# Optimization experiments

Measured on AMD Instinct MI355X. Metric: run time of the kernel, lower is better.

Reference implementation:

```python
import jax, jax.numpy as jnp
import numpy as np

BELIEF = 1024
STOCH = 32
DISC = 32
LATENT = 1024
MLP = 1024
ACT = 6
B = 256
T = 64
UNIMIX = 0.01
FREE = 0.1
DYN_SCALE = 1.0
REP_SCALE = 0.1
EPS = 1e-8
SAMP_EPS = 1e-6
CLIP = 20.0
UPDATE_BIAS = -1.0


def _lin_init(key, fan_in, fan_out):
    return jax.random.normal(key, (fan_in, fan_out), jnp.float32) / np.sqrt(fan_in)


def setup_inputs() -> dict:
    key = jax.random.key(0)
    ks = jax.random.split(key, 16)
    inp = {
        "b0": jnp.zeros((B, BELIEF), jnp.float32),
        "z0": jax.random.uniform(ks[0], (B, STOCH * DISC), jnp.float32),
        "actions": jax.random.normal(ks[1], (T, B, ACT), jnp.float32),
        "obs": jax.random.normal(ks[2], (T, B, LATENT), jnp.float32),
        "u_noise": jax.random.uniform(ks[3], (T, B, STOCH, DISC), jnp.float32),
        # imagine_in MLP: (stoch*disc + act) -> MLP -> LATENT
        "Wi1": _lin_init(ks[4], STOCH * DISC + ACT, MLP),
        "bi1": jnp.zeros((MLP,), jnp.float32),
        "Wi2": _lin_init(ks[5], MLP, LATENT),
        "bi2": jnp.zeros((LATENT,), jnp.float32),
        # GRU linear: (LATENT + BELIEF) -> 3*BELIEF, no bias; LayerNorm(3*BELIEF, eps=1e-3)
        "Wg": _lin_init(ks[6], LATENT + BELIEF, 3 * BELIEF),
        "ln_scale": jnp.ones((3 * BELIEF,), jnp.float32),
        "ln_bias": jnp.zeros((3 * BELIEF,), jnp.float32),
        # posterior MLP: (LATENT + BELIEF) -> LATENT -> STOCH*DISC
        "Wo1": _lin_init(ks[7], LATENT + BELIEF, LATENT),
        "bo1": jnp.zeros((LATENT,), jnp.float32),
        "Wo2": _lin_init(ks[8], LATENT, STOCH * DISC),
        "bo2": jnp.zeros((STOCH * DISC,), jnp.float32),
        # prior (belief decoder) MLP: BELIEF -> LATENT -> STOCH*DISC
        "Wp1": _lin_init(ks[9], BELIEF, LATENT),
        "bp1": jnp.zeros((LATENT,), jnp.float32),
        "Wp2": _lin_init(ks[10], LATENT, STOCH * DISC),
        "bp2": jnp.zeros((STOCH * DISC,), jnp.float32),
    }
    return inp


def _mlp2(x, W1, b1, W2, b2):
    h = jax.nn.silu(x @ W1 + b1)
    return h @ W2 + b2


def _layernorm(x, scale, bias, eps=1e-3):
    mu = x.mean(-1, keepdims=True)
    var = ((x - mu) ** 2).mean(-1, keepdims=True)
    return (x - mu) / jnp.sqrt(var + eps) * scale + bias


def _probs_from_logits(logits_flat):
    # reshape (..., STOCH*DISC) -> (..., STOCH, DISC), clip, softmax, unimix
    logits = logits_flat.reshape(*logits_flat.shape[:-1], STOCH, DISC)
    logits = jnp.clip(logits, -CLIP, CLIP)
    probs = jax.nn.softmax(logits, axis=-1)
    probs = probs * (1.0 - UNIMIX) + UNIMIX / DISC
    return probs


def _kl_cate(post_probs, prior_probs):
    sg = jax.lax.stop_gradient
    log_post = jnp.log(post_probs + EPS)
    kl_rep = (post_probs * (log_post - jnp.log(sg(prior_probs) + EPS))).sum((-2, -1))
    kl_dyn = (sg(post_probs) * (sg(log_post) - jnp.log(prior_probs + EPS))).sum((-2, -1))
    rep_loss = jnp.maximum(kl_rep, FREE)
    dyn_loss = jnp.maximum(kl_dyn, FREE)
    return DYN_SCALE * dyn_loss + REP_SCALE * rep_loss


def reference(b0, z0, actions, obs, u_noise,
              Wi1, bi1, Wi2, bi2,
              Wg, ln_scale, ln_bias,
              Wo1, bo1, Wo2, bo2,
              Wp1, bp1, Wp2, bp2):
    def gru(inp, h):
        gates = _layernorm(jnp.concatenate([inp, h], axis=-1) @ Wg, ln_scale, ln_bias)
        r, c, u = jnp.split(gates, 3, axis=-1)
        reset = jax.nn.sigmoid(r)
        cand = jnp.tanh(reset * c)
        update = jax.nn.sigmoid(u + UPDATE_BIAS)
        return update * cand + (1.0 - update) * h

    def step(carry, xs):
        b, z = carry
        a_t, o_t, u_t = xs
        inp = _mlp2(jnp.concatenate([z, a_t], axis=-1), Wi1, bi1, Wi2, bi2)
        b_new = gru(inp, b)                                      # (B, BELIEF)
        prior_probs = _probs_from_logits(_mlp2(b_new, Wp1, bp1, Wp2, bp2))
        post_probs = _probs_from_logits(
            _mlp2(jnp.concatenate([o_t, b_new], axis=-1), Wo1, bo1, Wo2, bo2))
        # gumbel-max categorical sample + straight-through one-hot
        g = -jnp.log(-jnp.log(u_t + SAMP_EPS) + SAMP_EPS)
        logp = jnp.log(jnp.maximum(post_probs, SAMP_EPS))
        hard = jnp.argmax(logp + g, axis=-1)                     # (B, STOCH)
        y_hard = jax.nn.one_hot(hard, DISC, dtype=post_probs.dtype)
        z_st = y_hard + post_probs - jax.lax.stop_gradient(post_probs)
        z_flat = z_st.reshape(z_st.shape[0], STOCH * DISC)
        loss = _kl_cate(post_probs, prior_probs)                 # (B,)
        return (b_new, z_flat), loss

    (_, _), losses = jax.lax.scan(step, (b0, z0), (actions, obs, u_noise))
    return losses  # (T, B)
```

## Files before the change

### kernel.cpp

```cpp
#include <hip/hip_runtime.h>
#include <math.h>


typedef _Float16 f16;
typedef _Float16 f16x8 __attribute__((ext_vector_type(8)));
typedef float f32x4 __attribute__((ext_vector_type(4)));

constexpr int kB = 256, kN1 = 1024, kG3N = 3072, kActD = 6, kT = 64;
constexpr float kLoScale = 4096.f;
constexpr float kLoInv = 1.f / 4096.f;

__device__ __forceinline__ float lda_sc(const float* p) {
  return __hip_atomic_load(p, __ATOMIC_RELAXED, __HIP_MEMORY_SCOPE_AGENT);
}
__device__ __forceinline__ void stg_sc(float* p, float v) {
  __hip_atomic_store(p, v, __ATOMIC_RELAXED, __HIP_MEMORY_SCOPE_AGENT);
}
__device__ __forceinline__ int aadd(int* p, int v) {
  return __hip_atomic_fetch_add(p, v, __ATOMIC_RELAXED, __HIP_MEMORY_SCOPE_AGENT);
}
__device__ __forceinline__ int ald(int* p) {
  return __hip_atomic_load(p, __ATOMIC_RELAXED, __HIP_MEMORY_SCOPE_AGENT);
}

__device__ __forceinline__ void wr_planes(f16* hi, f16* lo, size_t i, float x) {
  f16 h = (f16)x;
  hi[i] = h;
  lo[i] = (f16)((x - (float)h) * kLoScale);
}

__device__ __forceinline__ void glds16(const f16* g, f16* l) {
  __builtin_amdgcn_global_load_lds(
      (const __attribute__((address_space(1))) unsigned int*)g,
      (__attribute__((address_space(3))) unsigned int*)l, 16, 0, 0);
}

struct GemmLDS  { f16 As[3][2][8][64][8]; f16 Ws[3][2][4][64][8]; };
struct Gemm2LDS { f16 As[2][2][8][64][8]; f16 Ws[2][2][8][64][8]; };
struct GruLDS  { float sh[kG3N]; float red[8]; };
struct SmpLDS  { float skl[32]; int sidx[32]; };
union GGLDS { Gemm2LDS g; GruLDS r; };
union ESLDS { Gemm2LDS g; SmpLDS s; };

__device__ void dev_mgemm2(Gemm2LDS& L, const f16* A1h, const f16* A1l,
                           const f16* A2h, const f16* A2l,
                           const f16* Wph, const f16* Wpl, float* outF,
                           int cols1, int K, int Nout, int k0, int klen,
                           int bx, int byp, int pstride, int pidx) {
  const int m0 = bx * 128, n0 = byp * 128;
  const int tid = threadIdx.x, wave = tid >> 6, lane = tid & 63;
  const int rlo = lane & 15, khi = (lane >> 4) * 8;
  const int wmf = (wave & 1) * 4, wnf = (wave >> 1) * 4;

  f32x4 acc1[4][4], acc2[4][4];
#pragma unroll
  for (int i = 0; i < 4; ++i)
#pragma unroll
    for (int j = 0; j < 4; ++j)
#pragma unroll
      for (int r = 0; r < 4; ++r) { acc1[i][j][r] = 0.f; acc2[i][j][r] = 0.f; }

  auto issueTile = [&](int it, int buf) {
    const int kg = k0 + it * 32;
    const f16 *h, *l; int rs, cb;
    if (kg < cols1) { h = A1h; l = A1l; rs = cols1; cb = kg; }
    else { h = A2h; l = A2l; rs = K - cols1; cb = kg - cols1; }
#pragma unroll
    for (int i = 0; i < 2; ++i) {
      const int mf = wave * 2 + i;
      const size_t go = (size_t)(m0 + mf * 16 + rlo) * rs + cb + khi;
      glds16(h + go, &L.As[buf][0][mf][0][0]);
      glds16(l + go, &L.As[buf][1][mf][0][0]);
    }
#pragma unroll
    for (int i = 0; i < 2; ++i) {
      const int p = wave * 2 + i;
      const size_t wo = (size_t)(n0 + p * 16 + rlo) * K + kg + khi;
      glds16(Wph + wo, &L.Ws[buf][0][p][0][0]);
      glds16(Wpl + wo, &L.Ws[buf][1][p][0][0]);
    }
  };

  const int niter = klen >> 5;
  issueTile(0, 0);
#pragma unroll 1
  for (int it = 0; it < niter; ++it) {
    const int buf = it & 1;
    if (it + 1 < niter) {
      issueTile(it + 1, buf ^ 1);
      asm volatile("s_waitcnt vmcnt(8)" ::: "memory");
    } else {
      asm volatile("s_waitcnt vmcnt(0)" ::: "memory");
    }
    __builtin_amdgcn_s_barrier();
    asm volatile("" ::: "memory");
    f16x8 Af[4][2], Wf[4][2];
#pragma unroll
    for (int mf = 0; mf < 4; ++mf) {
      Af[mf][0] = *(const f16x8*)&L.As[buf][0][wmf + mf][lane][0];
      Af[mf][1] = *(const f16x8*)&L.As[buf][1][wmf + mf][lane][0];
    }
#pragma unroll
    for (int nf = 0; nf < 4; ++nf) {
      Wf[nf][0] = *(const f16x8*)&L.Ws[buf][0][wnf + nf][lane][0];
      Wf[nf][1] = *(const f16x8*)&L.Ws[buf][1][wnf + nf][lane][0];
    }
#pragma unroll
    for (int mf = 0; mf < 4; ++mf)
#pragma unroll
      for (int nf = 0; nf < 4; ++nf) {
        acc1[mf][nf] = __builtin_amdgcn_mfma_f32_16x16x32_f16(Af[mf][0], Wf[nf][0], acc1[mf][nf], 0, 0, 0);
        acc2[mf][nf] = __builtin_amdgcn_mfma_f32_16x16x32_f16(Af[mf][0], Wf[nf][1], acc2[mf][nf], 0, 0, 0);
        acc2[mf][nf] = __builtin_amdgcn_mfma_f32_16x16x32_f16(Af[mf][1], Wf[nf][0], acc2[mf][nf], 0, 0, 0);
      }
    __builtin_amdgcn_s_barrier();
  }
  __syncthreads();
  const int orow = m0 + (wave & 1) * 64, ocol = n0 + (wave >> 1) * 64;
#pragma unroll
  for (int mf = 0; mf < 4; ++mf)
#pragma unroll
    for (int nf = 0; nf < 4; ++nf)
#pragma unroll
      for (int r = 0; r < 4; ++r) {
        const int row = orow + mf * 16 + (lane >> 4) * 4 + r;
        const int col = ocol + nf * 16 + rlo;
        const int o = row * Nout + col;
        float* dst = outF + ((size_t)(o >> 4) * pstride + pidx) * 16 + (o & 15);
        stg_sc(dst, acc1[mf][nf][r] + acc2[mf][nf][r] * kLoInv);
      }
}

__device__ void dev_mgemm(GemmLDS& L, const f16* A1h, const f16* A1l,
                          const f16* A2h, const f16* A2l,
                          const f16* Wph, const f16* Wpl, float* outF,
                          int cols1, int K, int Nout, int k0, int klen,
                          int bx, int by, int pstride, int pidx) {
  const int m0 = bx * 128, n0 = by * 64;
  const int tid = threadIdx.x, wave = tid >> 6, lane = tid & 63;
  const int rlo = lane & 15, khi = (lane >> 4) * 8;
  const int wmf = (wave & 1) * 4, wnf = (wave >> 1) * 2;

  f32x4 acc1[4][2], acc2[4][2];
#pragma unroll
  for (int i = 0; i < 4; ++i)
#pragma unroll
    for (int j = 0; j < 2; ++j)
#pragma unroll
      for (int r = 0; r < 4; ++r) { acc1[i][j][r] = 0.f; acc2[i][j][r] = 0.f; }

  auto issueTile = [&](int it, int buf) {
    const int kg = k0 + it * 32;
    const f16 *h, *l; int rs, cb;
    if (kg < cols1) { h = A1h; l = A1l; rs = cols1; cb = kg; }
    else { h = A2h; l = A2l; rs = K - cols1; cb = kg - cols1; }
#pragma unroll
    for (int i = 0; i < 2; ++i) {
      const int mf = wave * 2 + i;
      const size_t go = (size_t)(m0 + mf * 16 + rlo) * rs + cb + khi;
      glds16(h + go, &L.As[buf][0][mf][0][0]);
      glds16(l + go, &L.As[buf][1][mf][0][0]);
    }
    const size_t wo = (size_t)(n0 + wave * 16 + rlo) * K + kg + khi;
    glds16(Wph + wo, &L.Ws[buf][0][wave][0][0]);
    glds16(Wpl + wo, &L.Ws[buf][1][wave][0][0]);
  };

  const int niter = klen >> 5;
  issueTile(0, 0);
  if (niter > 1) issueTile(1, 1);
#pragma unroll 1
  for (int it = 0; it < niter; ++it) {
    const int buf = it % 3;
    if (it + 1 < niter) {
      asm volatile("s_waitcnt vmcnt(6)" ::: "memory");
    } else {
      asm volatile("s_waitcnt vmcnt(0)" ::: "memory");
    }
    __builtin_amdgcn_s_barrier();
    asm volatile("" ::: "memory");
    if (it + 2 < niter) issueTile(it + 2, (it + 2) % 3);
    f16x8 Af[4][2], Wf[2][2];
#pragma unroll
    for (int mf = 0; mf < 4; ++mf) {
      Af[mf][0] = *(const f16x8*)&L.As[buf][0][wmf + mf][lane][0];
      Af[mf][1] = *(const f16x8*)&L.As[buf][1][wmf + mf][lane][0];
    }
#pragma unroll
    for (int nf = 0; nf < 2; ++nf) {
      Wf[nf][0] = *(const f16x8*)&L.Ws[buf][0][wnf + nf][lane][0];
      Wf[nf][1] = *(const f16x8*)&L.Ws[buf][1][wnf + nf][lane][0];
    }
#pragma unroll
    for (int mf = 0; mf < 4; ++mf)
#pragma unroll
      for (int nf = 0; nf < 2; ++nf) {
        acc1[mf][nf] = __builtin_amdgcn_mfma_f32_16x16x32_f16(Af[mf][0], Wf[nf][0], acc1[mf][nf], 0, 0, 0);
        acc2[mf][nf] = __builtin_amdgcn_mfma_f32_16x16x32_f16(Af[mf][0], Wf[nf][1], acc2[mf][nf], 0, 0, 0);
        acc2[mf][nf] = __builtin_amdgcn_mfma_f32_16x16x32_f16(Af[mf][1], Wf[nf][0], acc2[mf][nf], 0, 0, 0);
      }
  }
  __syncthreads();
  const int orow = m0 + (wave & 1) * 64, ocol = n0 + (wave >> 1) * 32;
#pragma unroll
  for (int mf = 0; mf < 4; ++mf)
#pragma unroll
    for (int nf = 0; nf < 2; ++nf)
#pragma unroll
      for (int r = 0; r < 4; ++r) {
        const int row = orow + mf * 16 + (lane >> 4) * 4 + r;
        const int col = ocol + nf * 16 + rlo;
        const int o = row * Nout + col;
        float* dst = outF + ((size_t)(o >> 4) * pstride + pidx) * 16 + (o & 15);
        stg_sc(dst, acc1[mf][nf][r] + acc2[mf][nf][r] * kLoInv);
      }
}

__device__ __forceinline__ void flag_bump(int* ctr) {
  asm volatile("s_waitcnt vmcnt(0)" ::: "memory");
  __syncthreads();
  if (threadIdx.x == 0) aadd(ctr, 1);
}
__device__ __forceinline__ void spin_ge(int* p, int tgt) {
  if (threadIdx.x == 0) {
    int guard = 0;
    while (ald(p) < tgt) {
      __builtin_amdgcn_s_sleep(4);
      if (++guard > (1 << 17)) break;
    }
  }
  __syncthreads();
}

__device__ __forceinline__ int permW(int B2, int pairsPerCls) {
  const int cls = B2 & 7, k = B2 >> 3;
  return ((cls * pairsPerCls + (k >> 1)) << 1) | (k & 1);
}

struct GGArgs {
  const f16 *h1h, *h1l, *bh_r, *bl_r;
  const f16 *WfTh, *WfTl, *WgBh, *WgBl;
  float* Pg;
  const float *bfused, *lns, *lnb, *obs;
  float* bbuf;
  f16 *bh_w, *bl_w, *onh, *onl;
  int* ctr;
  int t;
};

__global__ __launch_bounds__(256, 2) void k_gates_gru(GGArgs a) {
  __shared__ GGLDS L;
  const int t = a.t;
  if (blockIdx.x < 192) {
    const int task = permW(blockIdx.x, 12);
    const int j = task / 48, r = task % 48, bx = r & 1, byp = r >> 1;
    const bool top = (j < 2);
    dev_mgemm2(L.g, top ? a.h1h : a.bh_r, top ? a.h1l : a.bl_r, nullptr, nullptr,
               top ? a.WfTh : a.WgBh, top ? a.WfTl : a.WgBl,
               a.Pg, 1024, 1024, kG3N, (j & 1) * 512, 512, bx, byp, 4, j);
    flag_bump(a.ctr + bx * 16);
  }
  const int b = blockIdx.x;
  if (b >= kB) return;
  spin_ge(a.ctr + (b >> 7) * 16, (t + 1) * 96);

  GruLDS& G = L.r;
  const int tid = threadIdx.x;
  float v[12];
  float sum = 0.f, sq = 0.f;
#pragma unroll
  for (int i = 0; i < 12; ++i) {
    const int j = tid + i * 256;
    const size_t o = (size_t)b * kG3N + j;
    const float* base = a.Pg + ((o >> 4) * 4) * 16 + (o & 15);
    const float q0 = lda_sc(base),      q1 = lda_sc(base + 16);
    const float q2 = lda_sc(base + 32), q3 = lda_sc(base + 48);
    const float s = (((q0 + q1) + q2) + q3) + a.bfused[j];
    v[i] = s; sum += s; sq += s * s;
  }
  if (t < kT - 1) {
#pragma unroll
    for (int i = 0; i < 4; ++i) {
      const int j = tid + i * 256;
      wr_planes(a.onh, a.onl, (size_t)b * kN1 + j,
                a.obs[(size_t)(t + 1) * kB * kN1 + (size_t)b * kN1 + j]);
    }
  }
  for (int m = 1; m <= 32; m <<= 1) { sum += __shfl_xor(sum, m); sq += __shfl_xor(sq, m); }
  if ((tid & 63) == 0) { G.red[(tid >> 6) * 2] = sum; G.red[(tid >> 6) * 2 + 1] = sq; }
  __syncthreads();
  float ts = 0.f, tq = 0.f;
  for (int w = 0; w < 4; ++w) { ts += G.red[w * 2]; tq += G.red[w * 2 + 1]; }
  const float mu   = ts * (1.f / kG3N);
  const float var  = tq * (1.f / kG3N) - mu * mu;
  const float rinv = 1.f / sqrtf(var + 1e-3f);
#pragma unroll
  for (int i = 0; i < 12; ++i) {
    const int j = tid + i * 256;
    G.sh[j] = (v[i] - mu) * rinv * a.lns[j] + a.lnb[j];
  }
  __syncthreads();
#pragma unroll
  for (int i = 0; i < 4; ++i) {
    const int j = tid + i * 256;
    const float r = G.sh[j], c = G.sh[kN1 + j], u = G.sh[2 * kN1 + j];
    const float reset = 1.f / (1.f + expf(-r));
    const float cand  = tanhf(reset * c);
    const float upd   = 1.f / (1.f + expf(-(u - 1.f)));
    const size_t o = (size_t)b * kN1 + j;
    const float bn = upd * cand + (1.f - upd) * a.bbuf[o];
    a.bbuf[o] = bn;
    wr_planes(a.bh_w, a.bl_w, o, bn);
  }
}

struct DCArgs {
  const f16 *bh, *bl, *oth, *otl;
  const f16 *Wp1Th, *Wp1Tl, *Wo1Th, *Wo1Tl;
  float* PD;
  const float *bp1, *bo1;
  f16 *hph, *hpl, *hoh, *hol;
  int* ctr;
  int t;
};

__global__ __launch_bounds__(256, 2) void k_d_comb(DCArgs a) {
  __shared__ Gemm2LDS L;
  const int t = a.t;
  if (blockIdx.x < 96) {
    const int task = permW(blockIdx.x, 6);
    const int j = task >> 4, r = task & 15, bx = r & 1, byp = r >> 1;
    const f16 *Ah, *Al, *A2h = nullptr, *A2l = nullptr, *Wh, *Wl;
    int K, k0;
    if (j < 2) { Ah = a.bh; Al = a.bl; Wh = a.Wp1Th; Wl = a.Wp1Tl; K = 1024; k0 = j * 512; }
    else { Ah = a.oth; Al = a.otl; A2h = a.bh; A2l = a.bl; Wh = a.Wo1Th; Wl = a.Wo1Tl; K = 2048; k0 = (j - 2) * 512; }
    dev_mgemm2(L, Ah, Al, A2h, A2l, Wh, Wl, a.PD, 1024, K, kN1, k0, 512, bx, byp, 6, j);
    flag_bump(a.ctr + bx * 16);
  }
  spin_ge(a.ctr, (t + 1) * 48);
  spin_ge(a.ctr + 16, (t + 1) * 48);
#pragma unroll 1
  for (int idx = blockIdx.x; idx < 1024; idx += 192) {
    const int i = idx * 256 + (int)threadIdx.x;
    const float* base = a.PD + ((size_t)(i >> 4) * 6) * 16 + (i & 15);
    const float p0 = lda_sc(base),      p1 = lda_sc(base + 16);
    const float p2 = lda_sc(base + 32), p3 = lda_sc(base + 48);
    const float p4 = lda_sc(base + 64), p5 = lda_sc(base + 80);
    float sp = (p0 + p1) + a.bp1[i & (kN1 - 1)];
    sp = sp * (1.f / (1.f + expf(-sp)));
    wr_planes(a.hph, a.hpl, i, sp);
    float so = (((p2 + p3) + p4) + p5) + a.bo1[i & (kN1 - 1)];
    so = so * (1.f / (1.f + expf(-so)));
    wr_planes(a.hoh, a.hol, i, so);
  }
}

struct ESArgs {
  const f16 *hph, *hpl, *hoh, *hol;
  const f16 *Wp2Th, *Wp2Tl, *Wo2Th, *Wo2Tl;
  float* PE;
  const float *bp2, *bo2, *unz, *acts, *Wi1, *bi1;
  float* out;
  f16 *h1h, *h1l;
  int* ctr;
  int t;
};

__global__ __launch_bounds__(256, 2) void k_e_samp(ESArgs a) {
  __shared__ ESLDS L;
  const int t = a.t;
  if (blockIdx.x < 64) {
    const int task = permW(blockIdx.x, 4);
    const int j = task >> 4, r = task & 15, bx = r & 1, byp = r >> 1;
    const bool pr = (j < 2);
    dev_mgemm2(L.g, pr ? a.hph : a.hoh, pr ? a.hpl : a.hol, nullptr, nullptr,
               pr ? a.Wp2Th : a.Wo2Th, pr ? a.Wp2Tl : a.Wo2Tl,
               a.PE, 1024, 1024, kN1, (j & 1) * 512, 512, bx, byp, 4, j);
    flag_bump(a.ctr + bx * 16);
  }
  const int b = blockIdx.x;
  spin_ge(a.ctr + (b >> 7) * 16, (t + 1) * 32);

  SmpLDS& S = L.s;
  const int tid = threadIdx.x;
  const float* unz_t = a.unz + (size_t)t * kB * kN1;
  __syncthreads();
#pragma unroll
  for (int c = 0; c < 4; ++c) {
    const int j = c * 256 + tid;
    const int o = b * kN1 + j;
    const float* base = a.PE + ((size_t)(o >> 4) * 4) * 16 + (o & 15);
    const float e0 = lda_sc(base),      e1 = lda_sc(base + 16);
    const float e2 = lda_sc(base + 32), e3 = lda_sc(base + 48);
    float lp = e0 + e1 + a.bp2[j];
    float lo = e2 + e3 + a.bo2[j];
    lp = fminf(fmaxf(lp, -20.f), 20.f);
    lo = fminf(fmaxf(lo, -20.f), 20.f);
    float mp = lp, mo = lo;
    for (int m = 1; m <= 16; m <<= 1) { mp = fmaxf(mp, __shfl_xor(mp, m)); mo = fmaxf(mo, __shfl_xor(mo, m)); }
    const float ep = expf(lp - mp), eo = expf(lo - mo);
    float sp = ep, so = eo;
    for (int m = 1; m <= 16; m <<= 1) { sp += __shfl_xor(sp, m); so += __shfl_xor(so, m); }
    const float pp = (ep / sp) * 0.99f + (0.01f / 32.f);
    const float po = (eo / so) * 0.99f + (0.01f / 32.f);
    float kt = po * (logf(po + 1e-8f) - logf(pp + 1e-8f));
    for (int m = 1; m <= 16; m <<= 1) kt += __shfl_xor(kt, m);
    const float u = unz_t[o];
    const float g = -logf(-logf(u + 1e-6f) + 1e-6f);
    float vv = logf(fmaxf(po, 1e-6f)) + g;
    int ii = j & 31;
    for (int m = 1; m <= 16; m <<= 1) {
      const float vo = __shfl_xor(vv, m);
      const int   io = __shfl_xor(ii, m);
      if (vo > vv || (vo == vv && io < ii)) { vv = vo; ii = io; }
    }
    if ((tid & 31) == 0) { S.skl[j >> 5] = kt; S.sidx[j >> 5] = ii; }
  }
  __syncthreads();
  if (tid == 0) {
    float kl = 0.f;
    for (int gg = 0; gg < 32; ++gg) kl += S.skl[gg];
    const float dl = fmaxf(kl, 0.1f);
    a.out[(size_t)t * kB + b] = 1.0f * dl + 0.1f * dl;
  }
  if (t < kT - 1) {
    const float* act_next = a.acts + (size_t)(t + 1) * kB * kActD;
#pragma unroll
    for (int c = 0; c < 4; ++c) {
      const int j = c * 256 + tid;
      float s = a.bi1[j];
#pragma unroll
      for (int gg = 0; gg < 32; ++gg)
        s += a.Wi1[(size_t)(gg * 32 + S.sidx[gg]) * kN1 + j];
#pragma unroll
      for (int k = 0; k < kActD; ++k)
        s += act_next[b * kActD + k] * a.Wi1[(size_t)(kN1 + k) * kN1 + j];
      s = s * (1.f / (1.f + expf(-s)));
      wr_planes(a.h1h, a.h1l, (size_t)b * kN1 + j, s);
    }
  }
}

struct MJob {
  const f16 *A1h, *A1l, *A2h, *A2l;
  const f16 *Wph, *Wpl;
  float* outF;
  int cols1, K, Nout, k0, klen, ny, pstride, pidx;
};
struct MJobs { MJob j[6]; };

__global__ __launch_bounds__(256, 2) void k_mgemm(MJobs js) {
  const MJob jb = js.j[blockIdx.z];
  if ((int)blockIdx.y >= jb.ny) return;
  __shared__ GemmLDS L;
  dev_mgemm(L, jb.A1h, jb.A1l, jb.A2h, jb.A2l, jb.Wph, jb.Wpl, jb.outF,
            jb.cols1, jb.K, jb.Nout, jb.k0, jb.klen, blockIdx.x, blockIdx.y,
            jb.pstride, jb.pidx);
}

__global__ __launch_bounds__(256) void k_conv(const float* src, f16* dh, f16* dl) {
  const size_t i = (size_t)blockIdx.x * 256 + threadIdx.x;
  wr_planes(dh, dl, i, src[i]);
}

__global__ __launch_bounds__(256) void k_convT(const float* src, int rowoff, int srcN,
                                               int K, f16* dh, f16* dl) {
  __shared__ float T[64][65];
  const int k0 = blockIdx.x * 64, n0 = blockIdx.y * 64;
  const int tx = threadIdx.x & 63, ty = threadIdx.x >> 6;
#pragma unroll 4
  for (int i = 0; i < 16; ++i) {
    const int k = ty * 16 + i;
    T[k][tx] = src[(size_t)(rowoff + k0 + k) * srcN + n0 + tx];
  }
  __syncthreads();
#pragma unroll 4
  for (int i = 0; i < 16; ++i) {
    const int n = ty * 16 + i;
    const float x = T[tx][n];
    const size_t o = (size_t)(n0 + n) * K + k0 + tx;
    f16 h = (f16)x;
    dh[o] = h;
    dl[o] = (f16)((x - (float)h) * kLoScale);
  }
}

__global__ __launch_bounds__(256) void k_bfused(const float* Wg, const float* bi2, float* bf) {
  const int n = blockIdx.x * 256 + threadIdx.x;
  float s = 0.f;
#pragma unroll 16
  for (int j = 0; j < 1024; ++j) s += bi2[j] * Wg[(size_t)j * kG3N + n];
  bf[n] = s;
}

__global__ __launch_bounds__(256) void k_setup(const float* b0, float* bbuf, f16* bh, f16* bl) {
  const size_t i = (size_t)blockIdx.x * 256 + threadIdx.x;
  const float b = b0[i];
  bbuf[i] = b;
  wr_planes(bh, bl, i, b);
}

__global__ void k_zero(int* p) {
  const int i = blockIdx.x * 256 + threadIdx.x;
  if (i < 512) p[i] = 0;
}

__global__ __launch_bounds__(256) void k_finish0(const float* P, const float* Wi1,
    const float* bi1, const float* act0, f16* h1h, f16* h1l) {
  const int b = blockIdx.y;
  const int j = blockIdx.x * 256 + threadIdx.x;
  __shared__ float sact[kActD];
  if (threadIdx.x < kActD) sact[threadIdx.x] = act0[b * kActD + threadIdx.x];
  __syncthreads();
  float s = P[(size_t)b * kN1 + j] + bi1[j];
#pragma unroll
  for (int k = 0; k < kActD; ++k) s += sact[k] * Wi1[(size_t)(kN1 + k) * kN1 + j];
  s = s * (1.f / (1.f + expf(-s)));
  wr_planes(h1h, h1l, (size_t)b * kN1 + j, s);
}

extern "C" void kernel_launch(void* const* d_in, const int* in_sizes, int n_in,
                              void* d_out, int out_size, void* d_ws, size_t ws_size,
                              hipStream_t stream) {
  const float* b0   = (const float*)d_in[0];
  const float* z0   = (const float*)d_in[1];
  const float* acts = (const float*)d_in[2];
  const float* obs  = (const float*)d_in[3];
  const float* unz  = (const float*)d_in[4];
  const float* Wi1  = (const float*)d_in[5];
  const float* bi1  = (const float*)d_in[6];
  const float* Wi2  = (const float*)d_in[7];
  const float* bi2  = (const float*)d_in[8];
  const float* Wg   = (const float*)d_in[9];
  const float* lns  = (const float*)d_in[10];
  const float* lnb  = (const float*)d_in[11];
  const float* Wo1  = (const float*)d_in[12];
  const float* bo1  = (const float*)d_in[13];
  const float* Wo2  = (const float*)d_in[14];
  const float* bo2  = (const float*)d_in[15];
  const float* Wp1  = (const float*)d_in[16];
  const float* bp1  = (const float*)d_in[17];
  const float* Wp2  = (const float*)d_in[18];
  const float* bp2  = (const float*)d_in[19];
  float* out = (float*)d_out;

  char* wsb = (char*)d_ws;
  size_t off = 0;
  auto allocB = [&](size_t bytes) { char* p = wsb + off; off += (bytes + 255) & ~(size_t)255; return p; };
  const size_t PL = (size_t)kB * kN1;
  const size_t S3 = (size_t)kB * kG3N;
  const size_t W1 = (size_t)kN1 * kN1;

  float* Pg = (float*)allocB(4 * S3 * 4);
  float* Wfused_tmp = Pg;
  f16* WgTh = (f16*)allocB(W1 * 3 * 2);
  f16* WgTl = (f16*)allocB(W1 * 3 * 2);
  float* PD = (float*)WgTh;
  float* PE = (float*)WgTl;
  f16* h1h = (f16*)allocB(PL * 2);  f16* h1l = (f16*)allocB(PL * 2);
  f16* bh  = (f16*)allocB(PL * 2);  f16* bl  = (f16*)allocB(PL * 2);
  f16* hph = (f16*)allocB(PL * 2);  f16* hpl = (f16*)allocB(PL * 2);
  f16* hoh = (f16*)allocB(PL * 2);  f16* hol = (f16*)allocB(PL * 2);
  f16* o0h = (f16*)allocB(PL * 2);  f16* o0l = (f16*)allocB(PL * 2);
  f16* o1h = (f16*)allocB(PL * 2);  f16* o1l = (f16*)allocB(PL * 2);
  f16* z0h = (f16*)allocB(PL * 2);  f16* z0l = (f16*)allocB(PL * 2);
  float* bbuf   = (float*)allocB(PL * 4);
  float* bfused = (float*)allocB((size_t)kG3N * 4);
  f16* WfTh = (f16*)allocB(W1 * 3 * 2);  f16* WfTl = (f16*)allocB(W1 * 3 * 2);
  f16* WgBh = (f16*)allocB(W1 * 3 * 2);  f16* WgBl = (f16*)allocB(W1 * 3 * 2);
  f16* Wi2h = (f16*)allocB(W1 * 2);      f16* Wi2l = (f16*)allocB(W1 * 2);
  f16* Wi1Th = (f16*)allocB(W1 * 2);     f16* Wi1Tl = (f16*)allocB(W1 * 2);
  f16* Wo1Th = (f16*)allocB(W1 * 2 * 2); f16* Wo1Tl = (f16*)allocB(W1 * 2 * 2);
  f16* Wp1Th = (f16*)allocB(W1 * 2);     f16* Wp1Tl = (f16*)allocB(W1 * 2);
  f16* Wp2Th = (f16*)allocB(W1 * 2);     f16* Wp2Tl = (f16*)allocB(W1 * 2);
  f16* Wo2Th = (f16*)allocB(W1 * 2);     f16* Wo2Tl = (f16*)allocB(W1 * 2);
  int* cnt = (int*)allocB(4096);

  k_convT<<<dim3(16, 48), 256, 0, stream>>>(Wg, 0, kG3N, 1024, WgTh, WgTl);
  k_convT<<<dim3(16, 48), 256, 0, stream>>>(Wg, 1024, kG3N, 1024, WgBh, WgBl);
  k_convT<<<dim3(16, 16), 256, 0, stream>>>(Wi1, 0, kN1, 1024, Wi1Th, Wi1Tl);
  k_convT<<<dim3(32, 16), 256, 0, stream>>>(Wo1, 0, kN1, 2048, Wo1Th, Wo1Tl);
  k_convT<<<dim3(16, 16), 256, 0, stream>>>(Wp1, 0, kN1, 1024, Wp1Th, Wp1Tl);
  k_convT<<<dim3(16, 16), 256, 0, stream>>>(Wp2, 0, kN1, 1024, Wp2Th, Wp2Tl);
  k_convT<<<dim3(16, 16), 256, 0, stream>>>(Wo2, 0, kN1, 1024, Wo2Th, Wo2Tl);
  k_conv<<<dim3(4096), 256, 0, stream>>>(Wi2, Wi2h, Wi2l);
  k_bfused<<<dim3(12), 256, 0, stream>>>(Wg, bi2, bfused);
  {
    MJobs J{};
    J.j[0] = { Wi2h, Wi2l, nullptr, nullptr, WgTh, WgTl, Wfused_tmp, 1024, 1024, kG3N, 0, 1024, 48, 1, 0 };
    k_mgemm<<<dim3(8, 48, 1), 256, 0, stream>>>(J);
  }
  k_convT<<<dim3(16, 48), 256, 0, stream>>>(Wfused_tmp, 0, kG3N, 1024, WfTh, WfTl);
  k_setup<<<dim3(1024), 256, 0, stream>>>(b0, bbuf, bh, bl);
  k_conv<<<dim3(1024), 256, 0, stream>>>(z0, z0h, z0l);
  k_conv<<<dim3(1024), 256, 0, stream>>>(obs, o0h, o0l);
  k_zero<<<dim3(2), 256, 0, stream>>>(cnt);
  {
    MJobs J{};
    J.j[0] = { z0h, z0l, nullptr, nullptr, Wi1Th, Wi1Tl, PD, 1024, 1024, kN1, 0, 1024, 16, 1, 0 };
    k_mgemm<<<dim3(2, 16, 1), 256, 0, stream>>>(J);
  }
  k_finish0<<<dim3(4, kB), 256, 0, stream>>>(PD, Wi1, bi1, acts, h1h, h1l);

  for (int t = 0; t < kT; ++t) {
    f16* oth = (t & 1) ? o1h : o0h;
    f16* otl = (t & 1) ? o1l : o0l;
    f16* onh = (t & 1) ? o0h : o1h;
    f16* onl = (t & 1) ? o0l : o1l;

    GGArgs A;
    A.h1h = h1h; A.h1l = h1l; A.bh_r = bh; A.bl_r = bl;
    A.WfTh = WfTh; A.WfTl = WfTl; A.WgBh = WgBh; A.WgBl = WgBl;
    A.Pg = Pg; A.bfused = bfused; A.lns = lns; A.lnb = lnb; A.obs = obs;
    A.bbuf = bbuf; A.bh_w = bh; A.bl_w = bl; A.onh = onh; A.onl = onl;
    A.ctr = cnt; A.t = t;
    k_gates_gru<<<dim3(256), 256, 0, stream>>>(A);

    DCArgs D;
    D.bh = bh; D.bl = bl; D.oth = oth; D.otl = otl;
    D.Wp1Th = Wp1Th; D.Wp1Tl = Wp1Tl; D.Wo1Th = Wo1Th; D.Wo1Tl = Wo1Tl;
    D.PD = PD; D.bp1 = bp1; D.bo1 = bo1;
    D.hph = hph; D.hpl = hpl; D.hoh = hoh; D.hol = hol;
    D.ctr = cnt + 32; D.t = t;
    k_d_comb<<<dim3(192), 256, 0, stream>>>(D);

    ESArgs E;
    E.hph = hph; E.hpl = hpl; E.hoh = hoh; E.hol = hol;
    E.Wp2Th = Wp2Th; E.Wp2Tl = Wp2Tl; E.Wo2Th = Wo2Th; E.Wo2Tl = Wo2Tl;
    E.PE = PE; E.bp2 = bp2; E.bo2 = bo2; E.unz = unz; E.acts = acts;
    E.Wi1 = Wi1; E.bi1 = bi1; E.out = out; E.h1h = h1h; E.h1l = h1l;
    E.ctr = cnt + 64; E.t = t;
    k_e_samp<<<dim3(256), 256, 0, stream>>>(E);
  }
}
```

Measured before the change: 6.369 ms.

## Precompute obs projection for all steps and drop split-K partial reductions

The observation half of the posterior first-layer GEMM is hoisted out of the recurrence: all timesteps of obs are converted to f16 hi/lo planes and multiplied by the obs slice of Wo1 in one large batched GEMM before the loop. Each per-step GEMM now runs its full K range inside one block with 128x64 tiles, so it writes final outputs directly instead of split-K partials that a second phase had to sum. The posterior/prior first layer kernel no longer needs the counter-spin phase. The cost is fewer active blocks per step (96/64 instead of 192), longer serial K loops per block, and extra workspace for the full-sequence obs buffers.

Measured after the change: 13.59 ms. 113% more time.

```diff
diff --git a/kernel.cpp b/kernel.cpp
--- a/kernel.cpp
+++ b/kernel.cpp
@@ -35,186 +35,101 @@
       (__attribute__((address_space(3))) unsigned int*)l, 16, 0, 0);
 }
 
-struct GemmLDS  { f16 As[3][2][8][64][8]; f16 Ws[3][2][4][64][8]; };
-struct Gemm2LDS { f16 As[2][2][8][64][8]; f16 Ws[2][2][8][64][8]; };
+struct Core16LDS { f16 As[2][2][8][64][8]; f16 Ws[2][2][4][64][8]; };
+struct GemmLDS   { f16 As[3][2][8][64][8]; f16 Ws[3][2][4][64][8]; };
 struct GruLDS  { float sh[kG3N]; float red[8]; };
 struct SmpLDS  { float skl[32]; int sidx[32]; };
-union GGLDS { Gemm2LDS g; GruLDS r; };
-union ESLDS { Gemm2LDS g; SmpLDS s; };
-
-__device__ void dev_mgemm2(Gemm2LDS& L, const f16* A1h, const f16* A1l,
-                           const f16* A2h, const f16* A2l,
-                           const f16* Wph, const f16* Wpl, float* outF,
-                           int cols1, int K, int Nout, int k0, int klen,
-                           int bx, int byp, int pstride, int pidx) {
-  const int m0 = bx * 128, n0 = byp * 128;
+union GGLDS { Core16LDS g; GruLDS r; };
+union ESLDS { Core16LDS g; SmpLDS s; };
+
+__device__ __forceinline__ void gcore16(Core16LDS& L,
+    const f16* Ah, const f16* Al, int rsA,
+    const f16* Wh, const f16* Wl, int KW,
+    int kA, int kW, int m0, int n0,
+    f32x4 (&p)[4][2], bool accum) {
   const int tid = threadIdx.x, wave = tid >> 6, lane = tid & 63;
   const int rlo = lane & 15, khi = (lane >> 4) * 8;
-  const int wmf = (wave & 1) * 4, wnf = (wave >> 1) * 4;
-
-  f32x4 acc1[4][4], acc2[4][4];
+  const int wmf = (wave & 1) * 4, wnf = (wave >> 1) * 2;
+
+  f32x4 acc1[4][2], acc2[4][2];
 #pragma unroll
   for (int i = 0; i < 4; ++i)
 #pragma unroll
-    for (int j = 0; j < 4; ++j)
+    for (int j = 0; j < 2; ++j)
 #pragma unroll
       for (int r = 0; r < 4; ++r) { acc1[i][j][r] = 0.f; acc2[i][j][r] = 0.f; }
 
-  auto issueTile = [&](int it, int buf) {
-    const int kg = k0 + it * 32;
-    const f16 *h, *l; int rs, cb;
-    if (kg < cols1) { h = A1h; l = A1l; rs = cols1; cb = kg; }
-    else { h = A2h; l = A2l; rs = K - cols1; cb = kg - cols1; }
+  auto issue = [&](int it, int buf) {
+    const int kgA = kA + it * 32, kgW = kW + it * 32;
 #pragma unroll
     for (int i = 0; i < 2; ++i) {
       const int mf = wave * 2 + i;
-      const size_t go = (size_t)(m0 + mf * 16 + rlo) * rs + cb + khi;
-      glds16(h + go, &L.As[buf][0][mf][0][0]);
-      glds16(l + go, &L.As[buf][1][mf][0][0]);
-    }
-#pragma unroll
-    for (int i = 0; i < 2; ++i) {
-      const int p = wave * 2 + i;
-      const size_t wo = (size_t)(n0 + p * 16 + rlo) * K + kg + khi;
-      glds16(Wph + wo, &L.Ws[buf][0][p][0][0]);
-      glds16(Wpl + wo, &L.Ws[buf][1][p][0][0]);
-    }
+      const size_t go = (size_t)(m0 + mf * 16 + rlo) * rsA + kgA + khi;
+      glds16(Ah + go, &L.As[buf][0][mf][0][0]);
+      glds16(Al + go, &L.As[buf][1][mf][0][0]);
+    }
+    const size_t wo = (size_t)(n0 + wave * 16 + rlo) * KW + kgW + khi;
+    glds16(Wh + wo, &L.Ws[buf][0][wave][0][0]);
+    glds16(Wl + wo, &L.Ws[buf][1][wave][0][0]);
   };
 
-  const int niter = klen >> 5;
-  issueTile(0, 0);
+  issue(0, 0);
 #pragma unroll 1
-  for (int it = 0; it < niter; ++it) {
+  for (int it = 0; it < 16; ++it) {
     const int buf = it & 1;
-    if (it + 1 < niter) {
-      issueTile(it + 1, buf ^ 1);
-      asm volatile("s_waitcnt vmcnt(8)" ::: "memory");
+    if (it + 1 < 16) {
+      issue(it + 1, buf ^ 1);
+      asm volatile("s_waitcnt vmcnt(6)" ::: "memory");
     } else {
       asm volatile("s_waitcnt vmcnt(0)" ::: "memory");
     }
     __builtin_amdgcn_s_barrier();
     asm volatile("" ::: "memory");
-    f16x8 Af[4][2], Wf[4][2];
+    f16x8 Af[4][2], Wf[2][2];
 #pragma unroll
     for (int mf = 0; mf < 4; ++mf) {
       Af[mf][0] = *(const f16x8*)&L.As[buf][0][wmf + mf][lane][0];
       Af[mf][1] = *(const f16x8*)&L.As[buf][1][wmf + mf][lane][0];
     }
 #pragma unroll
-    for (int nf = 0; nf < 4; ++nf) {
+    for (int nf = 0; nf < 2; ++nf) {
       Wf[nf][0] = *(const f16x8*)&L.Ws[buf][0][wnf + nf][lane][0];
       Wf[nf][1] = *(const f16x8*)&L.Ws[buf][1][wnf + nf][lane][0];
     }
 #pragma unroll
     for (int mf = 0; mf < 4; ++mf)
 #pragma unroll
-      for (int nf = 0; nf < 4; ++nf) {
+      for (int nf = 0; nf < 2; ++nf) {
         acc1[mf][nf] = __builtin_amdgcn_mfma_f32_16x16x32_f16(Af[mf][0], Wf[nf][0], acc1[mf][nf], 0, 0, 0);
         acc2[mf][nf] = __builtin_amdgcn_mfma_f32_16x16x32_f16(Af[mf][0], Wf[nf][1], acc2[mf][nf], 0, 0, 0);
         acc2[mf][nf] = __builtin_amdgcn_mfma_f32_16x16x32_f16(Af[mf][1], Wf[nf][0], acc2[mf][nf], 0, 0, 0);
       }
     __builtin_amdgcn_s_barrier();
   }
-  __syncthreads();
-  const int orow = m0 + (wave & 1) * 64, ocol = n0 + (wave >> 1) * 64;
 #pragma unroll
   for (int mf = 0; mf < 4; ++mf)
 #pragma unroll
-    for (int nf = 0; nf < 4; ++nf)
+    for (int nf = 0; nf < 2; ++nf)
 #pragma unroll
       for (int r = 0; r < 4; ++r) {
-        const int row = orow + mf * 16 + (lane >> 4) * 4 + r;
-        const int col = ocol + nf * 16 + rlo;
-        const int o = row * Nout + col;
-        float* dst = outF + ((size_t)(o >> 4) * pstride + pidx) * 16 + (o & 15);
-        stg_sc(dst, acc1[mf][nf][r] + acc2[mf][nf][r] * kLoInv);
+        const float t = acc1[mf][nf][r] + acc2[mf][nf][r] * kLoInv;
+        p[mf][nf][r] = accum ? (p[mf][nf][r] + t) : t;
       }
 }
 
-__device__ void dev_mgemm(GemmLDS& L, const f16* A1h, const f16* A1l,
-                          const f16* A2h, const f16* A2l,
-                          const f16* Wph, const f16* Wpl, float* outF,
-                          int cols1, int K, int Nout, int k0, int klen,
-                          int bx, int by, int pstride, int pidx) {
-  const int m0 = bx * 128, n0 = by * 64;
-  const int tid = threadIdx.x, wave = tid >> 6, lane = tid & 63;
-  const int rlo = lane & 15, khi = (lane >> 4) * 8;
-  const int wmf = (wave & 1) * 4, wnf = (wave >> 1) * 2;
-
-  f32x4 acc1[4][2], acc2[4][2];
-#pragma unroll
-  for (int i = 0; i < 4; ++i)
-#pragma unroll
-    for (int j = 0; j < 2; ++j)
-#pragma unroll
-      for (int r = 0; r < 4; ++r) { acc1[i][j][r] = 0.f; acc2[i][j][r] = 0.f; }
-
-  auto issueTile = [&](int it, int buf) {
-    const int kg = k0 + it * 32;
-    const f16 *h, *l; int rs, cb;
-    if (kg < cols1) { h = A1h; l = A1l; rs = cols1; cb = kg; }
-    else { h = A2h; l = A2l; rs = K - cols1; cb = kg - cols1; }
-#pragma unroll
-    for (int i = 0; i < 2; ++i) {
-      const int mf = wave * 2 + i;
-      const size_t go = (size_t)(m0 + mf * 16 + rlo) * rs + cb + khi;
-      glds16(h + go, &L.As[buf][0][mf][0][0]);
-      glds16(l + go, &L.As[buf][1][mf][0][0]);
-    }
-    const size_t wo = (size_t)(n0 + wave * 16 + rlo) * K + kg + khi;
-    glds16(Wph + wo, &L.Ws[buf][0][wave][0][0]);
-    glds16(Wpl + wo, &L.Ws[buf][1][wave][0][0]);
-  };
-
-  const int niter = klen >> 5;
-  issueTile(0, 0);
-  if (niter > 1) issueTile(1, 1);
-#pragma unroll 1
-  for (int it = 0; it < niter; ++it) {
-    const int buf = it % 3;
-    if (it + 1 < niter) {
-      asm volatile("s_waitcnt vmcnt(6)" ::: "memory");
-    } else {
-      asm volatile("s_waitcnt vmcnt(0)" ::: "memory");
-    }
-    __builtin_amdgcn_s_barrier();
-    asm volatile("" ::: "memory");
-    if (it + 2 < niter) issueTile(it + 2, (it + 2) % 3);
-    f16x8 Af[4][2], Wf[2][2];
-#pragma unroll
-    for (int mf = 0; mf < 4; ++mf) {
-      Af[mf][0] = *(const f16x8*)&L.As[buf][0][wmf + mf][lane][0];
-      Af[mf][1] = *(const f16x8*)&L.As[buf][1][wmf + mf][lane][0];
-    }
-#pragma unroll
-    for (int nf = 0; nf < 2; ++nf) {
-      Wf[nf][0] = *(const f16x8*)&L.Ws[buf][0][wnf + nf][lane][0];
-      Wf[nf][1] = *(const f16x8*)&L.Ws[buf][1][wnf + nf][lane][0];
-    }
-#pragma unroll
-    for (int mf = 0; mf < 4; ++mf)
-#pragma unroll
-      for (int nf = 0; nf < 2; ++nf) {
-        acc1[mf][nf] = __builtin_amdgcn_mfma_f32_16x16x32_f16(Af[mf][0], Wf[nf][0], acc1[mf][nf], 0, 0, 0);
-        acc2[mf][nf] = __builtin_amdgcn_mfma_f32_16x16x32_f16(Af[mf][0], Wf[nf][1], acc2[mf][nf], 0, 0, 0);
-        acc2[mf][nf] = __builtin_amdgcn_mfma_f32_16x16x32_f16(Af[mf][1], Wf[nf][0], acc2[mf][nf], 0, 0, 0);
-      }
-  }
-  __syncthreads();
-  const int orow = m0 + (wave & 1) * 64, ocol = n0 + (wave >> 1) * 32;
-#pragma unroll
-  for (int mf = 0; mf < 4; ++mf)
-#pragma unroll
-    for (int nf = 0; nf < 2; ++nf)
-#pragma unroll
-      for (int r = 0; r < 4; ++r) {
-        const int row = orow + mf * 16 + (lane >> 4) * 4 + r;
-        const int col = ocol + nf * 16 + rlo;
-        const int o = row * Nout + col;
-        float* dst = outF + ((size_t)(o >> 4) * pstride + pidx) * 16 + (o & 15);
-        stg_sc(dst, acc1[mf][nf][r] + acc2[mf][nf][r] * kLoInv);
-      }
-}
+#define EPI_FOR(body)                                                    \
+  {                                                                      \
+    const int wave = threadIdx.x >> 6, lane = threadIdx.x & 63;          \
+    const int rlo = lane & 15;                                           \
+    const int orow = m0 + (wave & 1) * 64, ocol = n0 + (wave >> 1) * 32; \
+    _Pragma("unroll") for (int mf = 0; mf < 4; ++mf)                     \
+    _Pragma("unroll") for (int nf = 0; nf < 2; ++nf)                     \
+    _Pragma("unroll") for (int r = 0; r < 4; ++r) {                      \
+      const int row = orow + mf * 16 + (lane >> 4) * 4 + r;              \
+      const int col = ocol + nf * 16 + rlo;                              \
+      body                                                               \
+    }                                                                    \
+  }
 
 __device__ __forceinline__ void flag_bump(int* ctr) {
   asm volatile("s_waitcnt vmcnt(0)" ::: "memory");
@@ -232,37 +147,33 @@
   __syncthreads();
 }
 
-__device__ __forceinline__ int permW(int B2, int pairsPerCls) {
-  const int cls = B2 & 7, k = B2 >> 3;
-  return ((cls * pairsPerCls + (k >> 1)) << 1) | (k & 1);
-}
-
 struct GGArgs {
   const f16 *h1h, *h1l, *bh_r, *bl_r;
   const f16 *WfTh, *WfTl, *WgBh, *WgBl;
   float* Pg;
-  const float *bfused, *lns, *lnb, *obs;
+  const float *bfused, *lns, *lnb;
   float* bbuf;
-  f16 *bh_w, *bl_w, *onh, *onl;
+  f16 *bh_w, *bl_w;
   int* ctr;
   int t;
 };
 
-__global__ __launch_bounds__(256, 2) void k_gates_gru(GGArgs a) {
+__global__ __launch_bounds__(256, 1) void k_gates_gru(GGArgs a) {
   __shared__ GGLDS L;
   const int t = a.t;
-  if (blockIdx.x < 192) {
-    const int task = permW(blockIdx.x, 12);
-    const int j = task / 48, r = task % 48, bx = r & 1, byp = r >> 1;
-    const bool top = (j < 2);
-    dev_mgemm2(L.g, top ? a.h1h : a.bh_r, top ? a.h1l : a.bl_r, nullptr, nullptr,
-               top ? a.WfTh : a.WgBh, top ? a.WfTl : a.WgBl,
-               a.Pg, 1024, 1024, kG3N, (j & 1) * 512, 512, bx, byp, 4, j);
+  if (blockIdx.x < 96) {
+    const int bx = blockIdx.x & 1, by = blockIdx.x >> 1;
+    const int m0 = bx * 128, n0 = by * 64;
+    f32x4 p[4][2];
+    gcore16(L.g, a.h1h, a.h1l, 1024, a.WfTh, a.WfTl, 1024, 0,   0,   m0, n0, p, false);
+    gcore16(L.g, a.h1h, a.h1l, 1024, a.WfTh, a.WfTl, 1024, 512, 512, m0, n0, p, true);
+    gcore16(L.g, a.bh_r, a.bl_r, 1024, a.WgBh, a.WgBl, 1024, 0,   0,   m0, n0, p, true);
+    gcore16(L.g, a.bh_r, a.bl_r, 1024, a.WgBh, a.WgBl, 1024, 512, 512, m0, n0, p, true);
+    EPI_FOR({ stg_sc(a.Pg + (size_t)row * kG3N + col, p[mf][nf][r] + a.bfused[col]); })
     flag_bump(a.ctr + bx * 16);
   }
   const int b = blockIdx.x;
-  if (b >= kB) return;
-  spin_ge(a.ctr + (b >> 7) * 16, (t + 1) * 96);
+  spin_ge(a.ctr + (b >> 7) * 16, (t + 1) * 48);
 
   GruLDS& G = L.r;
   const int tid = threadIdx.x;
@@ -271,20 +182,8 @@
 #pragma unroll
   for (int i = 0; i < 12; ++i) {
     const int j = tid + i * 256;
-    const size_t o = (size_t)b * kG3N + j;
-    const float* base = a.Pg + ((o >> 4) * 4) * 16 + (o & 15);
-    const float q0 = lda_sc(base),      q1 = lda_sc(base + 16);
-    const float q2 = lda_sc(base + 32), q3 = lda_sc(base + 48);
-    const float s = (((q0 + q1) + q2) + q3) + a.bfused[j];
+    const float s = lda_sc(a.Pg + (size_t)b * kG3N + j);
     v[i] = s; sum += s; sq += s * s;
-  }
-  if (t < kT - 1) {
-#pragma unroll
-    for (int i = 0; i < 4; ++i) {
-      const int j = tid + i * 256;
-      wr_planes(a.onh, a.onl, (size_t)b * kN1 + j,
-                a.obs[(size_t)(t + 1) * kB * kN1 + (size_t)b * kN1 + j]);
-    }
   }
   for (int m = 1; m <= 32; m <<= 1) { sum += __shfl_xor(sum, m); sq += __shfl_xor(sq, m); }
   if ((tid & 63) == 0) { G.red[(tid >> 6) * 2] = sum; G.red[(tid >> 6) * 2 + 1] = sq; }
@@ -314,51 +213,45 @@
   }
 }
 
-struct DCArgs {
-  const f16 *bh, *bl, *oth, *otl;
+struct DPArgs {
+  const f16 *bh, *bl;
   const f16 *Wp1Th, *Wp1Tl, *Wo1Th, *Wo1Tl;
-  float* PD;
-  const float *bp1, *bo1;
+  const float *obs_pre, *bp1, *bo1;
   f16 *hph, *hpl, *hoh, *hol;
-  int* ctr;
   int t;
 };
 
-__global__ __launch_bounds__(256, 2) void k_d_comb(DCArgs a) {
-  __shared__ Gemm2LDS L;
+__global__ __launch_bounds__(256, 1) void k_dplanes(DPArgs a) {
+  __shared__ Core16LDS g;
   const int t = a.t;
-  if (blockIdx.x < 96) {
-    const int task = permW(blockIdx.x, 6);
-    const int j = task >> 4, r = task & 15, bx = r & 1, byp = r >> 1;
-    const f16 *Ah, *Al, *A2h = nullptr, *A2l = nullptr, *Wh, *Wl;
-    int K, k0;
-    if (j < 2) { Ah = a.bh; Al = a.bl; Wh = a.Wp1Th; Wl = a.Wp1Tl; K = 1024; k0 = j * 512; }
-    else { Ah = a.oth; Al = a.otl; A2h = a.bh; A2l = a.bl; Wh = a.Wo1Th; Wl = a.Wo1Tl; K = 2048; k0 = (j - 2) * 512; }
-    dev_mgemm2(L, Ah, Al, A2h, A2l, Wh, Wl, a.PD, 1024, K, kN1, k0, 512, bx, byp, 6, j);
-    flag_bump(a.ctr + bx * 16);
-  }
-  spin_ge(a.ctr, (t + 1) * 48);
-  spin_ge(a.ctr + 16, (t + 1) * 48);
-#pragma unroll 1
-  for (int idx = blockIdx.x; idx < 1024; idx += 192) {
-    const int i = idx * 256 + (int)threadIdx.x;
-    const float* base = a.PD + ((size_t)(i >> 4) * 6) * 16 + (i & 15);
-    const float p0 = lda_sc(base),      p1 = lda_sc(base + 16);
-    const float p2 = lda_sc(base + 32), p3 = lda_sc(base + 48);
-    const float p4 = lda_sc(base + 64), p5 = lda_sc(base + 80);
-    float sp = (p0 + p1) + a.bp1[i & (kN1 - 1)];
-    sp = sp * (1.f / (1.f + expf(-sp)));
-    wr_planes(a.hph, a.hpl, i, sp);
-    float so = (((p2 + p3) + p4) + p5) + a.bo1[i & (kN1 - 1)];
-    so = so * (1.f / (1.f + expf(-so)));
-    wr_planes(a.hoh, a.hol, i, so);
+  const int sub = blockIdx.x & 31, bx = sub & 1, by = sub >> 1;
+  const int m0 = bx * 128, n0 = by * 64;
+  const size_t PL = (size_t)kB * kN1;
+  f32x4 p[4][2];
+  if (blockIdx.x < 32) {
+    gcore16(g, a.bh, a.bl, 1024, a.Wp1Th, a.Wp1Tl, 1024, 0,   0,   m0, n0, p, false);
+    gcore16(g, a.bh, a.bl, 1024, a.Wp1Th, a.Wp1Tl, 1024, 512, 512, m0, n0, p, true);
+    EPI_FOR({
+      float s = p[mf][nf][r] + a.bp1[col];
+      s = s * (1.f / (1.f + expf(-s)));
+      wr_planes(a.hph, a.hpl, (size_t)row * kN1 + col, s);
+    })
+  } else {
+    gcore16(g, a.bh, a.bl, 1024, a.Wo1Th, a.Wo1Tl, 2048, 0, 1024, m0, n0, p, false);
+    EPI_FOR({ p[mf][nf][r] = a.obs_pre[t * PL + (size_t)row * kN1 + col] + p[mf][nf][r]; })
+    gcore16(g, a.bh, a.bl, 1024, a.Wo1Th, a.Wo1Tl, 2048, 512, 1536, m0, n0, p, true);
+    EPI_FOR({
+      float s = p[mf][nf][r] + a.bo1[col];
+      s = s * (1.f / (1.f + expf(-s)));
+      wr_planes(a.hoh, a.hol, (size_t)row * kN1 + col, s);
+    })
   }
 }
 
 struct ESArgs {
   const f16 *hph, *hpl, *hoh, *hol;
   const f16 *Wp2Th, *Wp2Tl, *Wo2Th, *Wo2Tl;
-  float* PE;
+  float *PEp, *PEo;
   const float *bp2, *bo2, *unz, *acts, *Wi1, *bi1;
   float* out;
   f16 *h1h, *h1l;
@@ -366,16 +259,22 @@
   int t;
 };
 
-__global__ __launch_bounds__(256, 2) void k_e_samp(ESArgs a) {
+__global__ __launch_bounds__(256, 1) void k_e_samp(ESArgs a) {
   __shared__ ESLDS L;
   const int t = a.t;
   if (blockIdx.x < 64) {
-    const int task = permW(blockIdx.x, 4);
-    const int j = task >> 4, r = task & 15, bx = r & 1, byp = r >> 1;
-    const bool pr = (j < 2);
-    dev_mgemm2(L.g, pr ? a.hph : a.hoh, pr ? a.hpl : a.hol, nullptr, nullptr,
-               pr ? a.Wp2Th : a.Wo2Th, pr ? a.Wp2Tl : a.Wo2Tl,
-               a.PE, 1024, 1024, kN1, (j & 1) * 512, 512, bx, byp, 4, j);
+    const int sub = blockIdx.x & 31, bx = sub & 1, by = sub >> 1;
+    const int m0 = bx * 128, n0 = by * 64;
+    f32x4 p[4][2];
+    if (blockIdx.x < 32) {
+      gcore16(L.g, a.hph, a.hpl, 1024, a.Wp2Th, a.Wp2Tl, 1024, 0,   0,   m0, n0, p, false);
+      gcore16(L.g, a.hph, a.hpl, 1024, a.Wp2Th, a.Wp2Tl, 1024, 512, 512, m0, n0, p, true);
+      EPI_FOR({ stg_sc(a.PEp + (size_t)row * kN1 + col, p[mf][nf][r] + a.bp2[col]); })
+    } else {
+      gcore16(L.g, a.hoh, a.hol, 1024, a.Wo2Th, a.Wo2Tl, 1024, 0,   0,   m0, n0, p, false);
+      gcore16(L.g, a.hoh, a.hol, 1024, a.Wo2Th, a.Wo2Tl, 1024, 512, 512, m0, n0, p, true);
+      EPI_FOR({ stg_sc(a.PEo + (size_t)row * kN1 + col, p[mf][nf][r] + a.bo2[col]); })
+    }
     flag_bump(a.ctr + bx * 16);
   }
   const int b = blockIdx.x;
@@ -389,11 +288,8 @@
   for (int c = 0; c < 4; ++c) {
     const int j = c * 256 + tid;
     const int o = b * kN1 + j;
-    const float* base = a.PE + ((size_t)(o >> 4) * 4) * 16 + (o & 15);
-    const float e0 = lda_sc(base),      e1 = lda_sc(base + 16);
-    const float e2 = lda_sc(base + 32), e3 = lda_sc(base + 48);
-    float lp = e0 + e1 + a.bp2[j];
-    float lo = e2 + e3 + a.bo2[j];
+    float lp = lda_sc(a.PEp + o);
+    float lo = lda_sc(a.PEo + o);
     lp = fminf(fmaxf(lp, -20.f), 20.f);
     lo = fminf(fmaxf(lo, -20.f), 20.f);
     float mp = lp, mo = lo;
@@ -441,11 +337,105 @@
   }
 }
 
+__global__ __launch_bounds__(256, 1) void k_obspre(const f16* oAh, const f16* oAl,
+    const f16* Wo1Th, const f16* Wo1Tl, float* obs_pre) {
+  __shared__ Core16LDS g;
+  const int bx = blockIdx.x >> 4, by = blockIdx.x & 15;
+  const int m0 = bx * 128, n0 = by * 64;
+  f32x4 p[4][2];
+  gcore16(g, oAh, oAl, 1024, Wo1Th, Wo1Tl, 2048, 0,   0,   m0, n0, p, false);
+  gcore16(g, oAh, oAl, 1024, Wo1Th, Wo1Tl, 2048, 512, 512, m0, n0, p, true);
+  EPI_FOR({ obs_pre[(size_t)row * kN1 + col] = p[mf][nf][r]; })
+}
+
+__device__ void dev_mgemm(GemmLDS& L, const f16* A1h, const f16* A1l,
+                          const f16* A2h, const f16* A2l,
+                          const f16* Wph, const f16* Wpl, float* outF,
+                          int cols1, int K, int Nout, int k0, int klen,
+                          int bx, int by) {
+  const int m0 = bx * 128, n0 = by * 64;
+  const int tid = threadIdx.x, wave = tid >> 6, lane = tid & 63;
+  const int rlo = lane & 15, khi = (lane >> 4) * 8;
+  const int wmf = (wave & 1) * 4, wnf = (wave >> 1) * 2;
+
+  f32x4 acc1[4][2], acc2[4][2];
+#pragma unroll
+  for (int i = 0; i < 4; ++i)
+#pragma unroll
+    for (int j = 0; j < 2; ++j)
+#pragma unroll
+      for (int r = 0; r < 4; ++r) { acc1[i][j][r] = 0.f; acc2[i][j][r] = 0.f; }
+
+  auto issueTile = [&](int it, int buf) {
+    const int kg = k0 + it * 32;
+    const f16 *h, *l; int rs, cb;
+    if (kg < cols1) { h = A1h; l = A1l; rs = cols1; cb = kg; }
+    else { h = A2h; l = A2l; rs = K - cols1; cb = kg - cols1; }
+#pragma unroll
+    for (int i = 0; i < 2; ++i) {
+      const int mf = wave * 2 + i;
+      const size_t go = (size_t)(m0 + mf * 16 + rlo) * rs + cb + khi;
+      glds16(h + go, &L.As[buf][0][mf][0][0]);
+      glds16(l + go, &L.As[buf][1][mf][0][0]);
+    }
+    const size_t wo = (size_t)(n0 + wave * 16 + rlo) * K + kg + khi;
+    glds16(Wph + wo, &L.Ws[buf][0][wave][0][0]);
+    glds16(Wpl + wo, &L.Ws[buf][1][wave][0][0]);
+  };
+
+  const int niter = klen >> 5;
+  issueTile(0, 0);
+  if (niter > 1) issueTile(1, 1);
+#pragma unroll 1
+  for (int it = 0; it < niter; ++it) {
+    const int buf = it % 3;
+    if (it + 1 < niter) {
+      asm volatile("s_waitcnt vmcnt(6)" ::: "memory");
+    } else {
+      asm volatile("s_waitcnt vmcnt(0)" ::: "memory");
+    }
+    __builtin_amdgcn_s_barrier();
+    asm volatile("" ::: "memory");
+    if (it + 2 < niter) issueTile(it + 2, (it + 2) % 3);
+    f16x8 Af[4][2], Wf[2][2];
+#pragma unroll
+    for (int mf = 0; mf < 4; ++mf) {
+      Af[mf][0] = *(const f16x8*)&L.As[buf][0][wmf + mf][lane][0];
+      Af[mf][1] = *(const f16x8*)&L.As[buf][1][wmf + mf][lane][0];
+    }
+#pragma unroll
+    for (int nf = 0; nf < 2; ++nf) {
+      Wf[nf][0] = *(const f16x8*)&L.Ws[buf][0][wnf + nf][lane][0];
+      Wf[nf][1] = *(const f16x8*)&L.Ws[buf][1][wnf + nf][lane][0];
+    }
+#pragma unroll
+    for (int mf = 0; mf < 4; ++mf)
+#pragma unroll
+      for (int nf = 0; nf < 2; ++nf) {
+        acc1[mf][nf] = __builtin_amdgcn_mfma_f32_16x16x32_f16(Af[mf][0], Wf[nf][0], acc1[mf][nf], 0, 0, 0);
+        acc2[mf][nf] = __builtin_amdgcn_mfma_f32_16x16x32_f16(Af[mf][0], Wf[nf][1], acc2[mf][nf], 0, 0, 0);
+        acc2[mf][nf] = __builtin_amdgcn_mfma_f32_16x16x32_f16(Af[mf][1], Wf[nf][0], acc2[mf][nf], 0, 0, 0);
+      }
+  }
+  __syncthreads();
+  const int orow = m0 + (wave & 1) * 64, ocol = n0 + (wave >> 1) * 32;
+#pragma unroll
+  for (int mf = 0; mf < 4; ++mf)
+#pragma unroll
+    for (int nf = 0; nf < 2; ++nf)
+#pragma unroll
+      for (int r = 0; r < 4; ++r) {
+        const int row = orow + mf * 16 + (lane >> 4) * 4 + r;
+        const int col = ocol + nf * 16 + rlo;
+        outF[(size_t)row * Nout + col] = acc1[mf][nf][r] + acc2[mf][nf][r] * kLoInv;
+      }
+}
+
 struct MJob {
   const f16 *A1h, *A1l, *A2h, *A2l;
   const f16 *Wph, *Wpl;
   float* outF;
-  int cols1, K, Nout, k0, klen, ny, pstride, pidx;
+  int cols1, K, Nout, k0, klen, ny;
 };
 struct MJobs { MJob j[6]; };
 
@@ -454,8 +444,7 @@
   if ((int)blockIdx.y >= jb.ny) return;
   __shared__ GemmLDS L;
   dev_mgemm(L, jb.A1h, jb.A1l, jb.A2h, jb.A2l, jb.Wph, jb.Wpl, jb.outF,
-            jb.cols1, jb.K, jb.Nout, jb.k0, jb.klen, blockIdx.x, blockIdx.y,
-            jb.pstride, jb.pidx);
+            jb.cols1, jb.K, jb.Nout, jb.k0, jb.klen, blockIdx.x, blockIdx.y);
 }
 
 __global__ __launch_bounds__(256) void k_conv(const float* src, f16* dh, f16* dl) {
@@ -548,21 +537,20 @@
   size_t off = 0;
   auto allocB = [&](size_t bytes) { char* p = wsb + off; off += (bytes + 255) & ~(size_t)255; return p; };
   const size_t PL = (size_t)kB * kN1;
-  const size_t S3 = (size_t)kB * kG3N;
   const size_t W1 = (size_t)kN1 * kN1;
-
-  float* Pg = (float*)allocB(4 * S3 * 4);
+  const size_t TPL = (size_t)kT * PL;
+
+  float* Pg = (float*)allocB((size_t)kB * kG3N * 4 * 4);
   float* Wfused_tmp = Pg;
   f16* WgTh = (f16*)allocB(W1 * 3 * 2);
   f16* WgTl = (f16*)allocB(W1 * 3 * 2);
-  float* PD = (float*)WgTh;
-  float* PE = (float*)WgTl;
+  float* PD  = (float*)WgTh;
+  float* PEp = (float*)WgTl;
+  float* PEo = PEp + PL;
   f16* h1h = (f16*)allocB(PL * 2);  f16* h1l = (f16*)allocB(PL * 2);
   f16* bh  = (f16*)allocB(PL * 2);  f16* bl  = (f16*)allocB(PL * 2);
   f16* hph = (f16*)allocB(PL * 2);  f16* hpl = (f16*)allocB(PL * 2);
   f16* hoh = (f16*)allocB(PL * 2);  f16* hol = (f16*)allocB(PL * 2);
-  f16* o0h = (f16*)allocB(PL * 2);  f16* o0l = (f16*)allocB(PL * 2);
-  f16* o1h = (f16*)allocB(PL * 2);  f16* o1l = (f16*)allocB(PL * 2);
   f16* z0h = (f16*)allocB(PL * 2);  f16* z0l = (f16*)allocB(PL * 2);
   float* bbuf   = (float*)allocB(PL * 4);
   float* bfused = (float*)allocB((size_t)kG3N * 4);
@@ -575,6 +563,9 @@
   f16* Wp2Th = (f16*)allocB(W1 * 2);     f16* Wp2Tl = (f16*)allocB(W1 * 2);
   f16* Wo2Th = (f16*)allocB(W1 * 2);     f16* Wo2Tl = (f16*)allocB(W1 * 2);
   int* cnt = (int*)allocB(4096);
+  f16* obsAh = (f16*)allocB(TPL * 2);
+  f16* obsAl = (f16*)allocB(TPL * 2);
+  float* obs_pre = (float*)allocB(TPL * 4);
 
   k_convT<<<dim3(16, 48), 256, 0, stream>>>(Wg, 0, kG3N, 1024, WgTh, WgTl);
   k_convT<<<dim3(16, 48), 256, 0, stream>>>(Wg, 1024, kG3N, 1024, WgBh, WgBl);
@@ -587,48 +578,45 @@
   k_bfused<<<dim3(12), 256, 0, stream>>>(Wg, bi2, bfused);
   {
     MJobs J{};
-    J.j[0] = { Wi2h, Wi2l, nullptr, nullptr, WgTh, WgTl, Wfused_tmp, 1024, 1024, kG3N, 0, 1024, 48, 1, 0 };
+    J.j[0] = { Wi2h, Wi2l, nullptr, nullptr, WgTh, WgTl, Wfused_tmp, 1024, 1024, kG3N, 0, 1024, 48 };
     k_mgemm<<<dim3(8, 48, 1), 256, 0, stream>>>(J);
   }
   k_convT<<<dim3(16, 48), 256, 0, stream>>>(Wfused_tmp, 0, kG3N, 1024, WfTh, WfTl);
+  k_conv<<<dim3(65536), 256, 0, stream>>>(obs, obsAh, obsAl);
+  k_obspre<<<dim3(2048), 256, 0, stream>>>(obsAh, obsAl, Wo1Th, Wo1Tl, obs_pre);
   k_setup<<<dim3(1024), 256, 0, stream>>>(b0, bbuf, bh, bl);
   k_conv<<<dim3(1024), 256, 0, stream>>>(z0, z0h, z0l);
-  k_conv<<<dim3(1024), 256, 0, stream>>>(obs, o0h, o0l);
   k_zero<<<dim3(2), 256, 0, stream>>>(cnt);
   {
     MJobs J{};
-    J.j[0] = { z0h, z0l, nullptr, nullptr, Wi1Th, Wi1Tl, PD, 1024, 1024, kN1, 0, 1024, 16, 1, 0 };
+    J.j[0] = { z0h, z0l, nullptr, nullptr, Wi1Th, Wi1Tl, PD, 1024, 1024, kN1, 0, 1024, 16 };
     k_mgemm<<<dim3(2, 16, 1), 256, 0, stream>>>(J);
   }
   k_finish0<<<dim3(4, kB), 256, 0, stream>>>(PD, Wi1, bi1, acts, h1h, h1l);
 
   for (int t = 0; t < kT; ++t) {
-    f16* oth = (t & 1) ? o1h : o0h;
-    f16* otl = (t & 1) ? o1l : o0l;
-    f16* onh = (t & 1) ? o0h : o1h;
-    f16* onl = (t & 1) ? o0l : o1l;
-
     GGArgs A;
     A.h1h = h1h; A.h1l = h1l; A.bh_r = bh; A.bl_r = bl;
     A.WfTh = WfTh; A.WfTl = WfTl; A.WgBh = WgBh; A.WgBl = WgBl;
-    A.Pg = Pg; A.bfused = bfused; A.lns = lns; A.lnb = lnb; A.obs = obs;
-    A.bbuf = bbuf; A.bh_w = bh; A.bl_w = bl; A.onh = onh; A.onl = onl;
+    A.Pg = Pg; A.bfused = bfused; A.lns = lns; A.lnb = lnb;
+    A.bbuf = bbuf; A.bh_w = bh; A.bl_w = bl;
     A.ctr = cnt; A.t = t;
     k_gates_gru<<<dim3(256), 256, 0, stream>>>(A);
 
-    DCArgs D;
-    D.bh = bh; D.bl = bl; D.oth = oth; D.otl = otl;
+    DPArgs D;
+    D.bh = bh; D.bl = bl;
     D.Wp1Th = Wp1Th; D.Wp1Tl = Wp1Tl; D.Wo1Th = Wo1Th; D.Wo1Tl = Wo1Tl;
-    D.PD = PD; D.bp1 = bp1; D.bo1 = bo1;
+    D.obs_pre = obs_pre; D.bp1 = bp1; D.bo1 = bo1;
     D.hph = hph; D.hpl = hpl; D.hoh = hoh; D.hol = hol;
-    D.ctr = cnt + 32; D.t = t;
-    k_d_comb<<<dim3(192), 256, 0, stream>>>(D);
+    D.t = t;
+    k_dplanes<<<dim3(64), 256, 0, stream>>>(D);
 
     ESArgs E;
     E.hph = hph; E.hpl = hpl; E.hoh = hoh; E.hol = hol;
     E.Wp2Th = Wp2Th; E.Wp2Tl = Wp2Tl; E.Wo2Th = Wo2Th; E.Wo2Tl = Wo2Tl;
-    E.PE = PE; E.bp2 = bp2; E.bo2 = bo2; E.unz = unz; E.acts = acts;
-    E.Wi1 = Wi1; E.bi1 = bi1; E.out = out; E.h1h = h1h; E.h1l = h1l;
+    E.PEp = PEp; E.PEo = PEo; E.bp2 = bp2; E.bo2 = bo2;
+    E.unz = unz; E.acts = acts; E.Wi1 = Wi1; E.bi1 = bi1;
+    E.out = out; E.h1h = h1h; E.h1l = h1l;
     E.ctr = cnt + 64; E.t = t;
     k_e_samp<<<dim3(256), 256, 0, stream>>>(E);
   }
```
